# Performance work log

Measured on AMD Instinct MI355X. Metric: run time of the kernel, lower is better.

Reference implementation:

```python
import jax, jax.numpy as jnp
import numpy as np

N, E, D, H, FF = 50000, 1600000, 128, 8, 512
DK = D // H
EPS = 1e-5


def _layernorm(x, g, b):
    mu = jnp.mean(x, axis=-1, keepdims=True)
    var = jnp.mean((x - mu) ** 2, axis=-1, keepdims=True)
    return (x - mu) * jax.lax.rsqrt(var + EPS) * g + b


def setup_inputs() -> dict:
    key = jax.random.key(0)
    ks = jax.random.split(key, 10)
    s = 0.05
    return {
        "h": jax.random.normal(ks[0], (N, D), jnp.float32),
        "src": jax.random.randint(ks[1], (E,), 0, N, jnp.int32),
        "dst": jax.random.randint(ks[2], (E,), 0, N, jnp.int32),
        "Wq": jax.random.normal(ks[3], (D, D), jnp.float32) * s,
        "Wk": jax.random.normal(ks[4], (D, D), jnp.float32) * s,
        "Wv": jax.random.normal(ks[5], (D, D), jnp.float32) * s,
        "Wo": jax.random.normal(ks[6], (D, D), jnp.float32) * s,
        "ln1_g": jnp.ones((D,), jnp.float32),
        "ln1_b": jnp.zeros((D,), jnp.float32),
        "ln2_g": jnp.ones((D,), jnp.float32),
        "ln2_b": jnp.zeros((D,), jnp.float32),
        "W1": jax.random.normal(ks[7], (D, FF), jnp.float32) * s,
        "b1": jnp.zeros((FF,), jnp.float32),
        "W2": jax.random.normal(ks[8], (FF, D), jnp.float32) * s,
        "b2": jnp.zeros((D,), jnp.float32),
    }


def reference(h, src, dst, Wq, Wk, Wv, Wo, ln1_g, ln1_b, ln2_g, ln2_b, W1, b1, W2, b2):
    # QKV projections (bias-free, as in the torch module)
    q = (h @ Wq).reshape(N, H, DK)
    k = (h @ Wk).reshape(N, H, DK)
    v = (h @ Wv).reshape(N, H, DK)

    # masked_mm: per-edge, per-head score  e[m,h] = q[dst[m]] . k[src[m]]
    e = jnp.einsum("ehd,ehd->eh", q[dst], k[src]) / np.sqrt(DK)

    # sparse_softmax: segment softmax over incoming edges of each dst node
    m = jax.ops.segment_max(e, dst, num_segments=N)  # [N, H]
    ex = jnp.exp(e - m[dst])
    denom = jax.ops.segment_sum(ex, dst, num_segments=N)  # [N, H]
    alpha = ex / denom[dst]  # [E, H]

    # vec_spmm: a[n] = sum_{edges m with dst[m]==n} alpha[m] * v[src[m]]
    a = jax.ops.segment_sum(alpha[:, :, None] * v[src], dst, num_segments=N)
    a = a.reshape(N, D)

    o = a @ Wo
    h1 = _layernorm(h + o, ln1_g, ln1_b)
    ffn = jax.nn.relu(h1 @ W1 + b1) @ W2 + b2
    h2 = _layernorm(h1 + ffn, ln2_g, ln2_b)
    return h2
```

## Files before the change

kernel.cpp:

```cpp
#include <hip/hip_runtime.h>
#include <hip/hip_bf16.h>
#include <math.h>

#define D   128
#define FFD 512
#define NPART 8
#define BINB 1024
#define BCAP 768
#define NPROD 32
#define NSUB 32
#define RCAP 320

typedef __attribute__((ext_vector_type(8))) short bf16x8;
typedef __attribute__((ext_vector_type(4))) float f32x4;
typedef __attribute__((ext_vector_type(2))) float f32x2;

static inline size_t align256(size_t x){ return (x + 255) & ~(size_t)255; }

__device__ __forceinline__ float bf2f(unsigned short u){
    union { unsigned int i; float f; } x; x.i = ((unsigned int)u) << 16; return x.f;
}
__device__ __forceinline__ unsigned short f2bf(float f){
    return __builtin_bit_cast(unsigned short, __float2bfloat16(f));
}
__device__ __forceinline__ unsigned char f2fp8(float f){
    return (unsigned char)(__builtin_amdgcn_cvt_pk_fp8_f32(f, f, 0, false) & 0xff);
}

#define DPP_ADD(x, ctrl) do { \
    int yi_ = __builtin_amdgcn_update_dpp(0, __builtin_bit_cast(int, x), ctrl, 0xf, 0xf, true); \
    x += __builtin_bit_cast(float, yi_); } while(0)

__global__ __launch_bounds__(256) void k_bin3(const int* __restrict__ src,
                                              const int* __restrict__ dst, int E, int N,
                                              unsigned long long* __restrict__ pairs,
                                              int* __restrict__ lens,
                                              unsigned long long* __restrict__ spill,
                                              int* __restrict__ qspill){
    __shared__ int lcur[8];
    int tid = threadIdx.x;
    if (tid < 8) lcur[tid] = 0;
    __syncthreads();
    int slice = (N + 7) >> 3;
    int T = gridDim.x * 256;
    unsigned long long* myreg = pairs + (size_t)blockIdx.x * 8 * BCAP;
    for (int i = blockIdx.x*256 + tid; i < E; i += T){
        int d = __builtin_nontemporal_load(&dst[i]);
        int s = __builtin_nontemporal_load(&src[i]);
        int b = min(d / slice, 7);
        unsigned long long pr = ((unsigned long long)(unsigned)d << 32) | (unsigned)s;
        int slot = atomicAdd(&lcur[b], 1);
        if (slot < BCAP) myreg[(size_t)b*BCAP + slot] = pr;
        else { int p = atomicAdd(qspill, 1); spill[p] = pr; }
    }
    __syncthreads();
    if (tid < 8) lens[blockIdx.x*8 + tid] = min(lcur[tid], BCAP);
}

__global__ __launch_bounds__(256) void k_rebin(const unsigned long long* __restrict__ pairs,
                                               const int* __restrict__ lens,
                                               unsigned* __restrict__ pairs2,
                                               int* __restrict__ rlens,
                                               unsigned long long* __restrict__ spill,
                                               int* __restrict__ qspill, int N){
    __shared__ int lcur[NSUB];
    int part = blockIdx.x & 7, ip = blockIdx.x >> 3;
    int tid = threadIdx.x;
    if (tid < NSUB) lcur[tid] = 0;
    __syncthreads();
    int slice = (N + 7) >> 3;
    unsigned subslice = (unsigned)(slice + NSUB - 1) / NSUB;
    int lo_part = part * slice;
    unsigned* outbase = pairs2 + (size_t)(part*NPROD + ip) * NSUB * RCAP;
    for (int seg = ip*(BINB/NPROD); seg < (ip+1)*(BINB/NPROD); ++seg){
        int len = lens[seg*8 + part];
        const unsigned long long* pp = pairs + ((size_t)seg*8 + part)*BCAP;
        for (int i = tid; i < len; i += 256){
            unsigned long long pr = pp[i];
            int d = (int)(pr >> 32);
            unsigned dl = (unsigned)(d - lo_part);
            unsigned sb = dl / subslice;
            int slot = atomicAdd(&lcur[sb], 1);
            if (slot < RCAP)
                outbase[(size_t)sb*RCAP + slot] = ((dl - sb*subslice) << 24) | (unsigned)pr & 0xFFFFFFu;
            else { int p = atomicAdd(qspill, 1); spill[p] = pr; }
        }
    }
    __syncthreads();
    if (tid < NSUB) rlens[(part*NPROD + ip)*NSUB + tid] = min(lcur[tid], RCAP);
}

__global__ __launch_bounds__(256) void k_count4(const unsigned* __restrict__ pairs2,
                                                const int* __restrict__ rlens,
                                                const unsigned long long* __restrict__ spill,
                                                const int* __restrict__ qspill,
                                                int* __restrict__ cnt, int N){
    __shared__ int hist[256];
    int part = blockIdx.x & 7, s = blockIdx.x >> 3;
    int slice = (N + 7) >> 3;
    int subslice = (slice + NSUB - 1) / NSUB;
    int lo_part = part*slice;
    int lo = lo_part + s*subslice;
    int part_end = min(lo_part + slice, N);
    int n_sub = max(0, min(subslice, part_end - lo));
    for (int i = threadIdx.x; i < 256; i += 256) hist[i] = 0;
    __syncthreads();
    for (int ip = 0; ip < NPROD; ++ip){
        int r = (part*NPROD + ip)*NSUB + s;
        int len = rlens[r];
        const unsigned* pp = pairs2 + (size_t)r*RCAP;
        for (int i = threadIdx.x; i < len; i += 256)
            atomicAdd(&hist[pp[i] >> 24], 1);
    }
    int ns = *qspill;
    for (int i = threadIdx.x; i < ns; i += 256){
        int r = (int)(spill[i] >> 32) - lo;
        if (r >= 0 && r < n_sub) atomicAdd(&hist[r], 1);
    }
    __syncthreads();
    for (int i = threadIdx.x; i < n_sub; i += 256) cnt[lo + i] = hist[i];
}

__global__ __launch_bounds__(256) void k_scatter4(const unsigned* __restrict__ pairs2,
                                                  const int* __restrict__ rlens,
                                                  const unsigned long long* __restrict__ spill,
                                                  const int* __restrict__ qspill,
                                                  const int* __restrict__ off,
                                                  int* __restrict__ csr_src, int N){
    __shared__ int curl[256];
    int part = blockIdx.x & 7, s = blockIdx.x >> 3;
    int slice = (N + 7) >> 3;
    int subslice = (slice + NSUB - 1) / NSUB;
    int lo_part = part*slice;
    int lo = lo_part + s*subslice;
    int part_end = min(lo_part + slice, N);
    int n_sub = max(0, min(subslice, part_end - lo));
    for (int i = threadIdx.x; i < n_sub; i += 256) curl[i] = off[lo + i];
    __syncthreads();
    for (int ip = 0; ip < NPROD; ++ip){
        int r = (part*NPROD + ip)*NSUB + s;
        int len = rlens[r];
        const unsigned* pp = pairs2 + (size_t)r*RCAP;
        for (int i = threadIdx.x; i < len; i += 256){
            unsigned e = pp[i];
            int pos = atomicAdd(&curl[e >> 24], 1);
            csr_src[pos] = (int)(e & 0xFFFFFFu);
        }
    }
    int ns = *qspill;
    for (int i = threadIdx.x; i < ns; i += 256){
        unsigned long long pr = spill[i];
        int r = (int)(pr >> 32) - lo;
        if (r >= 0 && r < n_sub){
            int pos = atomicAdd(&curl[r], 1);
            csr_src[pos] = (int)(unsigned)pr;
        }
    }
}

__global__ __launch_bounds__(256) void k_bsum(const int* __restrict__ cnt, int N,
                                              int* __restrict__ bsum){
    int id = blockIdx.x*256 + threadIdx.x;
    int v = (id < N) ? cnt[id] : 0;
    #pragma unroll
    for (int o = 1; o < 64; o <<= 1) v += __shfl_xor(v, o);
    __shared__ int w4[4];
    if ((threadIdx.x & 63) == 0) w4[threadIdx.x >> 6] = v;
    __syncthreads();
    if (threadIdx.x == 0) bsum[blockIdx.x] = w4[0] + w4[1] + w4[2] + w4[3];
}

__global__ __launch_bounds__(1024) void k_scanb(const int* __restrict__ bsum, int NB,
                                                int* __restrict__ ebase,
                                                int* __restrict__ off, int N){
    __shared__ int sh[1024];
    int tid = threadIdx.x;
    int v = (tid < NB) ? bsum[tid] : 0;
    sh[tid] = v; __syncthreads();
    for (int o = 1; o < 1024; o <<= 1){
        int t = (tid >= o) ? sh[tid-o] : 0;
        __syncthreads();
        sh[tid] += t;
        __syncthreads();
    }
    if (tid < NB) ebase[tid] = sh[tid] - v;
    if (tid == NB-1) off[N] = sh[tid];
}

__global__ __launch_bounds__(256) void k_off(const int* __restrict__ cnt, int N,
                                             const int* __restrict__ ebase,
                                             int* __restrict__ off){
    __shared__ int sh[256];
    int tid = threadIdx.x;
    int id = blockIdx.x*256 + tid;
    int v = (id < N) ? cnt[id] : 0;
    sh[tid] = v; __syncthreads();
    for (int o = 1; o < 256; o <<= 1){
        int t = (tid >= o) ? sh[tid-o] : 0;
        __syncthreads();
        sh[tid] += t;
        __syncthreads();
    }
    int excl = sh[tid] - v;
    int base = ebase[blockIdx.x];
    if (id < N) off[id] = base + excl;
}

__global__ __launch_bounds__(256) void k_cast(const float* __restrict__ x,
                                              __hip_bfloat16* __restrict__ y, int n4){
    int i = blockIdx.x*blockDim.x + threadIdx.x;
    if (i >= n4) return;
    float4 f = ((const float4*)x)[i];
    ushort4 u;
    u.x = f2bf(f.x); u.y = f2bf(f.y);
    u.z = f2bf(f.z); u.w = f2bf(f.w);
    ((ushort4*)y)[i] = u;
}

__global__ __launch_bounds__(256) void k_prep_all(
    const float* __restrict__ Wq, const float* __restrict__ Wk,
    const float* __restrict__ Wv, const float* __restrict__ Wo,
    const float* __restrict__ W1, const float* __restrict__ W2,
    __hip_bfloat16* __restrict__ Wqkvt, __hip_bfloat16* __restrict__ Wot,
    __hip_bfloat16* __restrict__ W1t,   __hip_bfloat16* __restrict__ W2t){
    const float* W; __hip_bfloat16* Wt; int K, Nc;
    int y = blockIdx.y;
    switch (y){
        case 0: W = Wq; Wt = Wqkvt; K = 128; Nc = 128; break;
        case 1: W = Wk; Wt = Wqkvt; K = 128; Nc = 128; break;
        case 2: W = Wv; Wt = Wqkvt; K = 128; Nc = 128; break;
        case 3: W = Wo; Wt = Wot;   K = 128; Nc = 128; break;
        case 4: W = W1; Wt = W1t;   K = 128; Nc = 512; break;
        default: W = W2; Wt = W2t;  K = 512; Nc = 128; break;
    }
    int total = K*Nc;
    for (int id = blockIdx.x*256 + threadIdx.x; id < total; id += 256*gridDim.x){
        int n = id / K, kk = id % K;
        size_t drow;
        if (y == 1)      drow = 128 + 8*(n>>2) + (n&3);
        else if (y == 2) drow = 128 + 8*(n>>2) + 4 + (n&3);
        else             drow = n;
        Wt[drow*K + kk] = __float2bfloat16(W[(size_t)kk*Nc + n]);
    }
}

#define BM 128
#define BN 128
#define BK 64

__device__ __forceinline__ bool tile_coords(int M, int &r0, int &c0){
    int ncols = gridDim.x;
    int f = blockIdx.y * ncols + blockIdx.x;
    int xcd = f & 7, s = f >> 3;
    int c = s % ncols, rl = s / ncols;
    int r = rl*8 + xcd;
    r0 = r*BM; c0 = c*BN;
    return r0 < M;
}

__device__ __forceinline__ void stage_tile(const __hip_bfloat16* __restrict__ src,
                                           int row_base, int row_limit, int ldK, int k0,
                                           __hip_bfloat16* lds){
    int tid = threadIdx.x;
    int wave = tid >> 6;
    #pragma unroll
    for (int i = 0; i < 4; ++i){
        int c = i*256 + tid;
        int r = c >> 3, s = c & 7;
        int sg = s ^ (r & 7);
        int gr = row_base + r; if (gr >= row_limit) gr = row_limit - 1;
        const __hip_bfloat16* gp = src + (size_t)gr*ldK + k0 + sg*8;
        char* lp = (char*)lds + (i*256 + wave*64)*16;
        __builtin_amdgcn_global_load_lds((const __attribute__((address_space(1))) void*)gp,
                                         (__attribute__((address_space(3))) void*)lp,
                                         16, 0, 0);
    }
}

__device__ __forceinline__ void stage_rows64(const __hip_bfloat16* __restrict__ src,
                                             int row_base, int ldK, int k0,
                                             __hip_bfloat16* lds){
    int tid = threadIdx.x;
    int wave = tid >> 6;
    #pragma unroll
    for (int i = 0; i < 2; ++i){
        int c = i*256 + tid;
        int r = c >> 3, s = c & 7;
        int sg = s ^ (r & 7);
        const __hip_bfloat16* gp = src + (size_t)(row_base + r)*ldK + k0 + sg*8;
        char* lp = (char*)lds + (i*256 + wave*64)*16;
        __builtin_amdgcn_global_load_lds((const __attribute__((address_space(1))) void*)gp,
                                         (__attribute__((address_space(3))) void*)lp,
                                         16, 0, 0);
    }
}

__device__ __forceinline__ bf16x8 frag(const __hip_bfloat16* buf, int R, int kk, int ls){
    int sl = (kk*4 + ls) ^ (R & 7);
    return *(const bf16x8*)((const char*)buf + R*128 + sl*16);
}

__global__ __launch_bounds__(256) void k_gemm_qkv(
    const __hip_bfloat16* __restrict__ A,
    const __hip_bfloat16* __restrict__ Bt,
    int M,
    __hip_bfloat16* __restrict__ qb, unsigned char* __restrict__ kvq){
    __shared__ __hip_bfloat16 As[BM*BK];
    __shared__ __hip_bfloat16 Bs[BN*BK];
    int r0, c0;
    if (!tile_coords(M, r0, c0)) return;
    int tid = threadIdx.x;
    int lane = tid & 63, wave = tid >> 6;
    int wr = wave >> 1, wc = wave & 1;
    int lr = lane & 15, ls = lane >> 4;

    f32x4 acc[4][4];
    #pragma unroll
    for (int m = 0; m < 4; m++)
        #pragma unroll
        for (int n = 0; n < 4; n++) acc[m][n] = (f32x4){0.f,0.f,0.f,0.f};

    for (int k0 = 0; k0 < 128; k0 += BK){
        stage_tile(A,  r0, M,   128, k0, As);
        stage_tile(Bt, c0, 384, 128, k0, Bs);
        __syncthreads();
        #pragma unroll
        for (int kk = 0; kk < 2; ++kk){
            bf16x8 af[4], bfg[4];
            #pragma unroll
            for (int m = 0; m < 4; m++) af[m]  = frag(As, wr*64 + m*16 + lr, kk, ls);
            #pragma unroll
            for (int n = 0; n < 4; n++) bfg[n] = frag(Bs, wc*64 + n*16 + lr, kk, ls);
            #pragma unroll
            for (int m = 0; m < 4; m++)
                #pragma unroll
                for (int n = 0; n < 4; n++)
                    acc[m][n] = __builtin_amdgcn_mfma_f32_16x16x32_bf16(af[m], bfg[n], acc[m][n], 0, 0, 0);
        }
        __syncthreads();
    }

    int region = c0 >> 7;
    #pragma unroll
    for (int n = 0; n < 4; n++){
        int c16 = wc*64 + n*16 + lr;
        #pragma unroll
        for (int m = 0; m < 4; m++){
            #pragma unroll
            for (int j = 0; j < 4; j++){
                int row = r0 + wr*64 + m*16 + ls*4 + j;
                if (row >= M) continue;
                float v = acc[m][n][j];
                if (region == 0)
                    ((unsigned short*)qb)[(size_t)row*128 + c16] = f2bf(v);
                else
                    kvq[(size_t)row*256 + (region-1)*128 + c16] = f2fp8(v);
            }
        }
    }
}

__global__ __launch_bounds__(256) void k_tail(
    const __hip_bfloat16* __restrict__ ab, const float* __restrict__ h,
    const __hip_bfloat16* __restrict__ Wot,
    const float* __restrict__ ln1g, const float* __restrict__ ln1b,
    const __hip_bfloat16* __restrict__ W1t, const float* __restrict__ b1,
    const __hip_bfloat16* __restrict__ W2t, const float* __restrict__ b2,
    const float* __restrict__ ln2g, const float* __restrict__ ln2b,
    float* __restrict__ out, int M){
    __shared__ __hip_bfloat16 buf0[BM*BK];
    __shared__ __hip_bfloat16 buf1[BM*BK];
    __shared__ __hip_bfloat16 h1s[2][BM*BK];
    __shared__ float red[2][BM][2];
    int f = blockIdx.x;
    int r0 = ((f >> 3)*8 + (f & 7)) * BM;
    if (r0 >= M) return;
    int tid = threadIdx.x;
    int lane = tid & 63, wave = tid >> 6;
    int wr = wave >> 1, wc = wave & 1;
    int lr = lane & 15, ls = lane >> 4;

    f32x4 acc[4][4];
    #pragma unroll
    for (int m = 0; m < 4; m++)
        #pragma unroll
        for (int n = 0; n < 4; n++) acc[m][n] = (f32x4){0.f,0.f,0.f,0.f};

    for (int k0 = 0; k0 < 128; k0 += BK){
        stage_tile(ab,  r0, M,   128, k0, buf0);
        stage_tile(Wot, 0,  128, 128, k0, buf1);
        __syncthreads();
        #pragma unroll
        for (int kk = 0; kk < 2; ++kk){
            bf16x8 af[4], bfg[4];
            #pragma unroll
            for (int m = 0; m < 4; m++) af[m]  = frag(buf0, wr*64 + m*16 + lr, kk, ls);
            #pragma unroll
            for (int n = 0; n < 4; n++) bfg[n] = frag(buf1, wc*64 + n*16 + lr, kk, ls);
            #pragma unroll
            for (int m = 0; m < 4; m++)
                #pragma unroll
                for (int n = 0; n < 4; n++)
                    acc[m][n] = __builtin_amdgcn_mfma_f32_16x16x32_bf16(af[m], bfg[n], acc[m][n], 0, 0, 0);
        }
        __syncthreads();
    }

    #pragma unroll
    for (int m = 0; m < 4; m++){
        #pragma unroll
        for (int j = 0; j < 4; j++){
            int rowl = wr*64 + m*16 + ls*4 + j;
            int row = r0 + rowl;
            float s = 0.f, q = 0.f;
            #pragma unroll
            for (int n = 0; n < 4; n++){
                int col = wc*64 + n*16 + lr;
                float rv = (row < M) ? h[(size_t)row*128 + col] : 0.f;
                float v = acc[m][n][j] + rv;
                acc[m][n][j] = v;
                s += v; q += v*v;
            }
            #pragma unroll
            for (int o = 1; o < 16; o <<= 1){
                s += __shfl_xor(s, o);
                q += __shfl_xor(q, o);
            }
            if (lr == 0){
                red[0][rowl][wc] = s;
                red[1][rowl][wc] = q;
            }
        }
    }
    __syncthreads();
    #pragma unroll
    for (int m = 0; m < 4; m++){
        #pragma unroll
        for (int j = 0; j < 4; j++){
            int rowl = wr*64 + m*16 + ls*4 + j;
            float mu  = (red[0][rowl][0] + red[0][rowl][1]) * (1.f/128.f);
            float eq  = (red[1][rowl][0] + red[1][rowl][1]) * (1.f/128.f);
            float var = fmaxf(eq - mu*mu, 0.f);
            float inv = rsqrtf(var + 1e-5f);
            #pragma unroll
            for (int n = 0; n < 4; n++){
                int col = wc*64 + n*16 + lr;
                float o = (acc[m][n][j] - mu)*inv*ln1g[col] + ln1b[col];
                int hh = col >> 6, c6 = col & 63;
                int slot = (c6 >> 3) ^ (rowl & 7), elem = c6 & 7;
                ((unsigned short*)h1s[hh])[rowl*64 + slot*8 + elem] = f2bf(o);
            }
        }
    }
    __syncthreads();

    f32x4 yacc[4][4];
    #pragma unroll
    for (int m = 0; m < 4; m++)
        #pragma unroll
        for (int n = 0; n < 4; n++) yacc[m][n] = (f32x4){0.f,0.f,0.f,0.f};

    for (int c = 0; c < 8; ++c){
        stage_rows64(W1t, c*64, 128, 0,  buf1);
        stage_rows64(W1t, c*64, 128, 64, buf1 + 64*64);
        __syncthreads();
        f32x4 tacc[4][2];
        #pragma unroll
        for (int m = 0; m < 4; m++)
            #pragma unroll
            for (int n = 0; n < 2; n++) tacc[m][n] = (f32x4){0.f,0.f,0.f,0.f};
        #pragma unroll
        for (int step = 0; step < 2; ++step){
            #pragma unroll
            for (int kk = 0; kk < 2; ++kk){
                bf16x8 af[4], bfg[2];
                #pragma unroll
                for (int m = 0; m < 4; m++) af[m]  = frag(h1s[step], wr*64 + m*16 + lr, kk, ls);
                #pragma unroll
                for (int n = 0; n < 2; n++) bfg[n] = frag(buf1 + step*64*64, wc*32 + n*16 + lr, kk, ls);
                #pragma unroll
                for (int m = 0; m < 4; m++)
                    #pragma unroll
                    for (int n = 0; n < 2; n++)
                        tacc[m][n] = __builtin_amdgcn_mfma_f32_16x16x32_bf16(af[m], bfg[n], tacc[m][n], 0, 0, 0);
            }
        }
        #pragma unroll
        for (int m = 0; m < 4; m++){
            #pragma unroll
            for (int j = 0; j < 4; j++){
                int rowl = wr*64 + m*16 + ls*4 + j;
                #pragma unroll
                for (int n = 0; n < 2; n++){
                    int cc = wc*32 + n*16 + lr;
                    float v = fmaxf(tacc[m][n][j] + b1[c*64 + cc], 0.f);
                    int slot = (cc >> 3) ^ (rowl & 7), elem = cc & 7;
                    ((unsigned short*)buf0)[rowl*64 + slot*8 + elem] = f2bf(v);
                }
            }
        }
        __syncthreads();
        stage_tile(W2t, 0, 128, 512, c*64, buf1);
        __syncthreads();
        #pragma unroll
        for (int kk = 0; kk < 2; ++kk){
            bf16x8 af[4], bfg[4];
            #pragma unroll
            for (int m = 0; m < 4; m++) af[m]  = frag(buf0, wr*64 + m*16 + lr, kk, ls);
            #pragma unroll
            for (int n = 0; n < 4; n++) bfg[n] = frag(buf1, wc*64 + n*16 + lr, kk, ls);
            #pragma unroll
            for (int m = 0; m < 4; m++)
                #pragma unroll
                for (int n = 0; n < 4; n++)
                    yacc[m][n] = __builtin_amdgcn_mfma_f32_16x16x32_bf16(af[m], bfg[n], yacc[m][n], 0, 0, 0);
        }
        __syncthreads();
    }

    #pragma unroll
    for (int m = 0; m < 4; m++){
        #pragma unroll
        for (int j = 0; j < 4; j++){
            int rowl = wr*64 + m*16 + ls*4 + j;
            float s = 0.f, q = 0.f;
            #pragma unroll
            for (int n = 0; n < 4; n++){
                int col = wc*64 + n*16 + lr;
                int hh = col >> 6, c6 = col & 63;
                int slot = (c6 >> 3) ^ (rowl & 7), elem = c6 & 7;
                float h1v = bf2f(((const unsigned short*)h1s[hh])[rowl*64 + slot*8 + elem]);
                float v = yacc[m][n][j] + b2[col] + h1v;
                yacc[m][n][j] = v;
                s += v; q += v*v;
            }
            #pragma unroll
            for (int o = 1; o < 16; o <<= 1){
                s += __shfl_xor(s, o);
                q += __shfl_xor(q, o);
            }
            if (lr == 0){
                red[0][rowl][wc] = s;
                red[1][rowl][wc] = q;
            }
        }
    }
    __syncthreads();
    #pragma unroll
    for (int m = 0; m < 4; m++){
        #pragma unroll
        for (int j = 0; j < 4; j++){
            int rowl = wr*64 + m*16 + ls*4 + j;
            int row = r0 + rowl;
            if (row >= M) continue;
            float mu  = (red[0][rowl][0] + red[0][rowl][1]) * (1.f/128.f);
            float eq  = (red[1][rowl][0] + red[1][rowl][1]) * (1.f/128.f);
            float var = fmaxf(eq - mu*mu, 0.f);
            float inv = rsqrtf(var + 1e-5f);
            #pragma unroll
            for (int n = 0; n < 4; n++){
                int col = wc*64 + n*16 + lr;
                out[(size_t)row*128 + col] = (yacc[m][n][j] - mu)*inv*ln2g[col] + ln2b[col];
            }
        }
    }
}

#define PAIR(jj, dd, b0, b1, b2, b3) { \
    int s0_ = __builtin_amdgcn_readlane(myidx, (jj)); \
    int s1_ = __builtin_amdgcn_readlane(myidx, (jj)+1); \
    int sv_ = half ? s1_ : s0_; \
    uint2 u_ = kv[(size_t)(unsigned)sv_*32 + l32]; \
    f32x2 k01 = __builtin_amdgcn_cvt_pk_f32_fp8((int)u_.x, false); \
    f32x2 k23 = __builtin_amdgcn_cvt_pk_f32_fp8((int)u_.x, true); \
    f32x2 v01 = __builtin_amdgcn_cvt_pk_f32_fp8((int)u_.y, false); \
    f32x2 v23 = __builtin_amdgcn_cvt_pk_f32_fp8((int)u_.y, true); \
    float p_ = q0*k01[0] + q1*k01[1] + q2*k23[0] + q3*k23[1]; \
    DPP_ADD(p_, 0xB1); DPP_ADD(p_, 0x4E); \
    float w_ = __builtin_amdgcn_exp2f(p_); \
    dd += w_; \
    b0 = fmaf(w_, v01[0], b0); b1 = fmaf(w_, v01[1], b1); \
    b2 = fmaf(w_, v23[0], b2); b3 = fmaf(w_, v23[1], b3); }

#define PAIRV(jj, dd, b0, b1, b2, b3) { \
    int s0_ = __builtin_amdgcn_readlane(myidx, (jj)); \
    int s1_ = __builtin_amdgcn_readlane(myidx, min((jj)+1, 63)); \
    int sv_ = half ? s1_ : s0_; \
    uint2 u_ = kv[(size_t)(unsigned)sv_*32 + l32]; \
    f32x2 k01 = __builtin_amdgcn_cvt_pk_f32_fp8((int)u_.x, false); \
    f32x2 k23 = __builtin_amdgcn_cvt_pk_f32_fp8((int)u_.x, true); \
    f32x2 v01 = __builtin_amdgcn_cvt_pk_f32_fp8((int)u_.y, false); \
    f32x2 v23 = __builtin_amdgcn_cvt_pk_f32_fp8((int)u_.y, true); \
    float p_ = q0*k01[0] + q1*k01[1] + q2*k23[0] + q3*k23[1]; \
    DPP_ADD(p_, 0xB1); DPP_ADD(p_, 0x4E); \
    float w_ = __builtin_amdgcn_exp2f(p_); \
    if ((jj) + half >= cnt) w_ = 0.f; \
    dd += w_; \
    b0 = fmaf(w_, v01[0], b0); b1 = fmaf(w_, v01[1], b1); \
    b2 = fmaf(w_, v23[0], b2); b3 = fmaf(w_, v23[1], b3); }

__global__ __launch_bounds__(256) void k_attn(const __hip_bfloat16* __restrict__ qb,
                                              const uint2* __restrict__ kv,
                                              const int* __restrict__ off,
                                              const int* __restrict__ csr_src,
                                              __hip_bfloat16* __restrict__ a, int N){
    int wid = (blockIdx.x*blockDim.x + threadIdx.x) >> 6;
    int lane = threadIdx.x & 63;
    if (wid >= N) return;
    int half = lane >> 5, l32 = lane & 31;
    ushort4 qu = ((const ushort4*)(qb + (size_t)wid*128))[l32];
    const float SC = 0.25f * 1.44269504f;
    float q0 = bf2f(qu.x)*SC, q1 = bf2f(qu.y)*SC, q2 = bf2f(qu.z)*SC, q3 = bf2f(qu.w)*SC;
    int beg = off[wid], end = off[wid+1];
    float dA=0, a0A=0, a1A=0, a2A=0, a3A=0;
    float dB=0, a0B=0, a1B=0, a2B=0, a3B=0;
    for (int e0 = beg; e0 < end; e0 += 64){
        int myidx = (e0 + lane < end) ? csr_src[e0 + lane] : 0;
        int cnt = min(64, end - e0);
        int j = 0;
        for (; j + 3 < cnt; j += 4){
            PAIR(j,   dA, a0A, a1A, a2A, a3A);
            PAIR(j+2, dB, a0B, a1B, a2B, a3B);
        }
        for (; j < cnt; j += 2){
            PAIRV(j, dA, a0A, a1A, a2A, a3A);
        }
    }
    float d  = dA + dB;
    float a0 = a0A + a0B, a1 = a1A + a1B, a2 = a2A + a2B, a3 = a3A + a3B;
    d  += __shfl_xor(d, 32);
    a0 += __shfl_xor(a0, 32);
    a1 += __shfl_xor(a1, 32);
    a2 += __shfl_xor(a2, 32);
    a3 += __shfl_xor(a3, 32);
    if (half == 0){
        float r = (d > 0.f) ? 1.f/d : 0.f;
        ushort4 o;
        o.x = f2bf(a0*r); o.y = f2bf(a1*r); o.z = f2bf(a2*r); o.w = f2bf(a3*r);
        ((ushort4*)(a + (size_t)wid*128))[l32] = o;
    }
}

extern "C" void kernel_launch(void* const* d_in, const int* in_sizes, int n_in,
                              void* d_out, int out_size, void* d_ws, size_t ws_size,
                              hipStream_t stream){
    const float* h    = (const float*)d_in[0];
    const int*   src  = (const int*)  d_in[1];
    const int*   dst  = (const int*)  d_in[2];
    const float* Wq   = (const float*)d_in[3];
    const float* Wk   = (const float*)d_in[4];
    const float* Wv   = (const float*)d_in[5];
    const float* Wo   = (const float*)d_in[6];
    const float* ln1g = (const float*)d_in[7];
    const float* ln1b = (const float*)d_in[8];
    const float* ln2g = (const float*)d_in[9];
    const float* ln2b = (const float*)d_in[10];
    const float* W1   = (const float*)d_in[11];
    const float* b1   = (const float*)d_in[12];
    const float* W2   = (const float*)d_in[13];
    const float* b2   = (const float*)d_in[14];
    float* out = (float*)d_out;

    const int N = in_sizes[0] / D;
    const int E = in_sizes[1];

    char* ws = (char*)d_ws;
    size_t o = 0;
    const size_t row_bf = align256((size_t)N * D * sizeof(__hip_bfloat16));
    const size_t kv_q   = align256((size_t)N * 256);

    __hip_bfloat16* qb  = (__hip_bfloat16*)(ws + o); o += row_bf;
    unsigned char* kvq  = (unsigned char*)(ws + o); o += kv_q;
    __hip_bfloat16* ab  = (__hip_bfloat16*)(ws + o); o += row_bf;
    __hip_bfloat16* hb  = (__hip_bfloat16*)(ws + o); o += row_bf;
    __hip_bfloat16* Wqkvt = (__hip_bfloat16*)(ws + o); o += align256(384*128*2);
    __hip_bfloat16* W1t   = (__hip_bfloat16*)(ws + o); o += align256(512*128*2);
    __hip_bfloat16* W2t   = (__hip_bfloat16*)(ws + o); o += align256(128*512*2);
    __hip_bfloat16* Wot   = (__hip_bfloat16*)(ws + o); o += align256(128*128*2);
    int* cnt   = (int*)(ws + o); o += align256((size_t)N*4);
    int* offp  = (int*)(ws + o); o += align256((size_t)(N+1)*4);
    int* bsum  = (int*)(ws + o); o += align256(1024*4);
    int* ebase = (int*)(ws + o); o += align256(1024*4);
    int* lens  = (int*)(ws + o); o += align256((size_t)BINB*8*4);
    int* rlens = (int*)(ws + o); o += align256((size_t)NPART*NPROD*NSUB*4);
    int* qspill= (int*)(ws + o); o += align256(256);
    int* csr   = (int*)(ws + o); o += align256((size_t)E*4);
    unsigned long long* pairs = (unsigned long long*)(ws + o);
    o += align256((size_t)BINB * 8 * BCAP * 8);
    unsigned* pairs2 = (unsigned*)(ws + o);
    o += align256((size_t)NPART * NPROD * NSUB * RCAP * 4);
    unsigned long long* spill = (unsigned long long*)(ws + o);
    o += align256((size_t)E * 8);

    const int NB = (N + 255)/256;

    (void)hipMemsetAsync(qspill, 0, 256, stream);
    k_bin3<<<BINB, 256, 0, stream>>>(src, dst, E, N, pairs, lens, spill, qspill);

    k_cast<<<(N*D/4 + 255)/256, 256, 0, stream>>>(h, hb, N*D/4);
    k_prep_all<<<dim3(64, 6), 256, 0, stream>>>(Wq, Wk, Wv, Wo, W1, W2,
                                                Wqkvt, Wot, W1t, W2t);

    k_rebin<<<NPART*NPROD, 256, 0, stream>>>(pairs, lens, pairs2, rlens, spill, qspill, N);
    k_count4<<<NPART*NSUB, 256, 0, stream>>>(pairs2, rlens, spill, qspill, cnt, N);
    k_bsum <<<NB, 256, 0, stream>>>(cnt, N, bsum);
    k_scanb<<<1, 1024, 0, stream>>>(bsum, NB, ebase, offp, N);
    k_off  <<<NB, 256, 0, stream>>>(cnt, N, ebase, offp);
    k_scatter4<<<NPART*NSUB, 256, 0, stream>>>(pairs2, rlens, spill, qspill, offp, csr, N);

    int mb = (N + BM - 1)/BM;
    int mb_pad = ((mb + 7)/8)*8;

    k_gemm_qkv<<<dim3(3, mb_pad), 256, 0, stream>>>(hb, Wqkvt, N, qb, kvq);

    k_attn<<<(N*64 + 255)/256, 256, 0, stream>>>(qb, (const uint2*)kvq, offp, csr, ab, N);

    k_tail<<<mb_pad, 256, 0, stream>>>(ab, h, Wot, ln1g, ln1b,
                                       W1t, b1, W2t, b2, ln2g, ln2b, out, N);
}
```

Baseline: 235.3 us.

## Use 512-thread blocks in fused tail kernel with 8-wave column split

The fused tail kernel (Wo projection, LayerNorm, FFN, LayerNorm) moves from 4 waves to 8 waves per 128-row block. Each wave now owns 32 output columns, or 16 FFN hidden columns, instead of twice that, and the row-statistic reductions combine four partial sums per row. Shared memory is merged into one 64KB buffer, with the reduction scratch aliased onto the first staging buffer, and the staging helpers are rewritten for 512 threads. The aim is more waves in flight to hide latency and smaller per-wave accumulators. The cost is that each wave reuses its A-fragments across fewer MFMAs and the same LDS fragment loads are repeated across more waves.

```diff
diff --git a/kernel.cpp b/kernel.cpp
--- a/kernel.cpp
+++ b/kernel.cpp
@@ -277,22 +277,38 @@
     }
 }
 
-__device__ __forceinline__ void stage_rows64(const __hip_bfloat16* __restrict__ src,
-                                             int row_base, int ldK, int k0,
-                                             __hip_bfloat16* lds){
+__device__ __forceinline__ void stage_tile512(const __hip_bfloat16* __restrict__ src,
+                                              int row_base, int row_limit, int ldK, int k0,
+                                              __hip_bfloat16* lds){
     int tid = threadIdx.x;
     int wave = tid >> 6;
     #pragma unroll
     for (int i = 0; i < 2; ++i){
-        int c = i*256 + tid;
+        int c = i*512 + tid;
         int r = c >> 3, s = c & 7;
         int sg = s ^ (r & 7);
-        const __hip_bfloat16* gp = src + (size_t)(row_base + r)*ldK + k0 + sg*8;
-        char* lp = (char*)lds + (i*256 + wave*64)*16;
+        int gr = row_base + r; if (gr >= row_limit) gr = row_limit - 1;
+        const __hip_bfloat16* gp = src + (size_t)gr*ldK + k0 + sg*8;
+        char* lp = (char*)lds + (i*512 + wave*64)*16;
         __builtin_amdgcn_global_load_lds((const __attribute__((address_space(1))) void*)gp,
                                          (__attribute__((address_space(3))) void*)lp,
                                          16, 0, 0);
     }
+}
+
+__device__ __forceinline__ void stage_rows64_512(const __hip_bfloat16* __restrict__ src,
+                                                 int row_base, int ldK, int k0,
+                                                 __hip_bfloat16* lds){
+    int tid = threadIdx.x;
+    int wave = tid >> 6;
+    int c = tid;
+    int r = c >> 3, s = c & 7;
+    int sg = s ^ (r & 7);
+    const __hip_bfloat16* gp = src + (size_t)(row_base + r)*ldK + k0 + sg*8;
+    char* lp = (char*)lds + (wave*64)*16;
+    __builtin_amdgcn_global_load_lds((const __attribute__((address_space(1))) void*)gp,
+                                     (__attribute__((address_space(3))) void*)lp,
+                                     16, 0, 0);
 }
 
 __device__ __forceinline__ bf16x8 frag(const __hip_bfloat16* buf, int R, int kk, int ls){
@@ -360,7 +376,7 @@
     }
 }
 
-__global__ __launch_bounds__(256) void k_tail(
+__global__ __launch_bounds__(512) void k_tail(
     const __hip_bfloat16* __restrict__ ab, const float* __restrict__ h,
     const __hip_bfloat16* __restrict__ Wot,
     const float* __restrict__ ln1g, const float* __restrict__ ln1b,
@@ -368,39 +384,42 @@
     const __hip_bfloat16* __restrict__ W2t, const float* __restrict__ b2,
     const float* __restrict__ ln2g, const float* __restrict__ ln2b,
     float* __restrict__ out, int M){
-    __shared__ __hip_bfloat16 buf0[BM*BK];
-    __shared__ __hip_bfloat16 buf1[BM*BK];
-    __shared__ __hip_bfloat16 h1s[2][BM*BK];
-    __shared__ float red[2][BM][2];
+    __shared__ char smem[65536];
+    __hip_bfloat16* buf0 = (__hip_bfloat16*)smem;
+    __hip_bfloat16* buf1 = (__hip_bfloat16*)(smem + 16384);
+    __hip_bfloat16* h1s0 = (__hip_bfloat16*)(smem + 32768);
+    __hip_bfloat16* h1s1 = (__hip_bfloat16*)(smem + 49152);
+    float* red0 = (float*)smem;
+    float* red1 = (float*)(smem + 2048);
     int f = blockIdx.x;
     int r0 = ((f >> 3)*8 + (f & 7)) * BM;
     if (r0 >= M) return;
     int tid = threadIdx.x;
     int lane = tid & 63, wave = tid >> 6;
-    int wr = wave >> 1, wc = wave & 1;
+    int wr = wave >> 2, wq = wave & 3;
     int lr = lane & 15, ls = lane >> 4;
 
-    f32x4 acc[4][4];
+    f32x4 acc[4][2];
     #pragma unroll
     for (int m = 0; m < 4; m++)
         #pragma unroll
-        for (int n = 0; n < 4; n++) acc[m][n] = (f32x4){0.f,0.f,0.f,0.f};
+        for (int n = 0; n < 2; n++) acc[m][n] = (f32x4){0.f,0.f,0.f,0.f};
 
     for (int k0 = 0; k0 < 128; k0 += BK){
-        stage_tile(ab,  r0, M,   128, k0, buf0);
-        stage_tile(Wot, 0,  128, 128, k0, buf1);
+        stage_tile512(ab,  r0, M,   128, k0, buf0);
+        stage_tile512(Wot, 0,  128, 128, k0, buf1);
         __syncthreads();
         #pragma unroll
         for (int kk = 0; kk < 2; ++kk){
-            bf16x8 af[4], bfg[4];
+            bf16x8 af[4], bfg[2];
             #pragma unroll
             for (int m = 0; m < 4; m++) af[m]  = frag(buf0, wr*64 + m*16 + lr, kk, ls);
             #pragma unroll
-            for (int n = 0; n < 4; n++) bfg[n] = frag(buf1, wc*64 + n*16 + lr, kk, ls);
+            for (int n = 0; n < 2; n++) bfg[n] = frag(buf1, wq*32 + n*16 + lr, kk, ls);
             #pragma unroll
             for (int m = 0; m < 4; m++)
                 #pragma unroll
-                for (int n = 0; n < 4; n++)
+                for (int n = 0; n < 2; n++)
                     acc[m][n] = __builtin_amdgcn_mfma_f32_16x16x32_bf16(af[m], bfg[n], acc[m][n], 0, 0, 0);
         }
         __syncthreads();
@@ -414,8 +433,8 @@
             int row = r0 + rowl;
             float s = 0.f, q = 0.f;
             #pragma unroll
-            for (int n = 0; n < 4; n++){
-                int col = wc*64 + n*16 + lr;
+            for (int n = 0; n < 2; n++){
+                int col = wq*32 + n*16 + lr;
                 float rv = (row < M) ? h[(size_t)row*128 + col] : 0.f;
                 float v = acc[m][n][j] + rv;
                 acc[m][n][j] = v;
@@ -427,8 +446,8 @@
                 q += __shfl_xor(q, o);
             }
             if (lr == 0){
-                red[0][rowl][wc] = s;
-                red[1][rowl][wc] = q;
+                red0[rowl*4 + wq] = s;
+                red1[rowl*4 + wq] = q;
             }
         }
     }
@@ -438,51 +457,49 @@
         #pragma unroll
         for (int j = 0; j < 4; j++){
             int rowl = wr*64 + m*16 + ls*4 + j;
-            float mu  = (red[0][rowl][0] + red[0][rowl][1]) * (1.f/128.f);
-            float eq  = (red[1][rowl][0] + red[1][rowl][1]) * (1.f/128.f);
-            float var = fmaxf(eq - mu*mu, 0.f);
+            float s4 = red0[rowl*4+0] + red0[rowl*4+1] + red0[rowl*4+2] + red0[rowl*4+3];
+            float q4 = red1[rowl*4+0] + red1[rowl*4+1] + red1[rowl*4+2] + red1[rowl*4+3];
+            float mu  = s4 * (1.f/128.f);
+            float var = fmaxf(q4 * (1.f/128.f) - mu*mu, 0.f);
             float inv = rsqrtf(var + 1e-5f);
             #pragma unroll
-            for (int n = 0; n < 4; n++){
-                int col = wc*64 + n*16 + lr;
+            for (int n = 0; n < 2; n++){
+                int col = wq*32 + n*16 + lr;
                 float o = (acc[m][n][j] - mu)*inv*ln1g[col] + ln1b[col];
-                int hh = col >> 6, c6 = col & 63;
+                int c6 = col & 63;
                 int slot = (c6 >> 3) ^ (rowl & 7), elem = c6 & 7;
-                ((unsigned short*)h1s[hh])[rowl*64 + slot*8 + elem] = f2bf(o);
-            }
-        }
-    }
-    __syncthreads();
-
-    f32x4 yacc[4][4];
+                unsigned short* dstp = (unsigned short*)((col >> 6) ? h1s1 : h1s0);
+                dstp[rowl*64 + slot*8 + elem] = f2bf(o);
+            }
+        }
+    }
+    __syncthreads();
+
+    f32x4 yacc[4][2];
     #pragma unroll
     for (int m = 0; m < 4; m++)
         #pragma unroll
-        for (int n = 0; n < 4; n++) yacc[m][n] = (f32x4){0.f,0.f,0.f,0.f};
+        for (int n = 0; n < 2; n++) yacc[m][n] = (f32x4){0.f,0.f,0.f,0.f};
 
     for (int c = 0; c < 8; ++c){
-        stage_rows64(W1t, c*64, 128, 0,  buf1);
-        stage_rows64(W1t, c*64, 128, 64, buf1 + 64*64);
-        __syncthreads();
-        f32x4 tacc[4][2];
-        #pragma unroll
-        for (int m = 0; m < 4; m++)
-            #pragma unroll
-            for (int n = 0; n < 2; n++) tacc[m][n] = (f32x4){0.f,0.f,0.f,0.f};
+        stage_rows64_512(W1t, c*64, 128, 0,  buf1);
+        stage_rows64_512(W1t, c*64, 128, 64, buf1 + 64*64);
+        __syncthreads();
+        f32x4 tacc[4];
+        #pragma unroll
+        for (int m = 0; m < 4; m++) tacc[m] = (f32x4){0.f,0.f,0.f,0.f};
         #pragma unroll
         for (int step = 0; step < 2; ++step){
+            const __hip_bfloat16* hs = step ? h1s1 : h1s0;
             #pragma unroll
             for (int kk = 0; kk < 2; ++kk){
-                bf16x8 af[4], bfg[2];
+                bf16x8 af[4], bw;
                 #pragma unroll
-                for (int m = 0; m < 4; m++) af[m]  = frag(h1s[step], wr*64 + m*16 + lr, kk, ls);
-                #pragma unroll
-                for (int n = 0; n < 2; n++) bfg[n] = frag(buf1 + step*64*64, wc*32 + n*16 + lr, kk, ls);
+                for (int m = 0; m < 4; m++) af[m] = frag(hs, wr*64 + m*16 + lr, kk, ls);
+                bw = frag(buf1 + step*64*64, wq*16 + lr, kk, ls);
                 #pragma unroll
                 for (int m = 0; m < 4; m++)
-                    #pragma unroll
-                    for (int n = 0; n < 2; n++)
-                        tacc[m][n] = __builtin_amdgcn_mfma_f32_16x16x32_bf16(af[m], bfg[n], tacc[m][n], 0, 0, 0);
+                    tacc[m] = __builtin_amdgcn_mfma_f32_16x16x32_bf16(af[m], bw, tacc[m], 0, 0, 0);
             }
         }
         #pragma unroll
@@ -490,29 +507,26 @@
             #pragma unroll
             for (int j = 0; j < 4; j++){
                 int rowl = wr*64 + m*16 + ls*4 + j;
-                #pragma unroll
-                for (int n = 0; n < 2; n++){
-                    int cc = wc*32 + n*16 + lr;
-                    float v = fmaxf(tacc[m][n][j] + b1[c*64 + cc], 0.f);
-                    int slot = (cc >> 3) ^ (rowl & 7), elem = cc & 7;
-                    ((unsigned short*)buf0)[rowl*64 + slot*8 + elem] = f2bf(v);
-                }
-            }
-        }
-        __syncthreads();
-        stage_tile(W2t, 0, 128, 512, c*64, buf1);
+                int cc = wq*16 + lr;
+                float v = fmaxf(tacc[m][j] + b1[c*64 + cc], 0.f);
+                int slot = (cc >> 3) ^ (rowl & 7), elem = cc & 7;
+                ((unsigned short*)buf0)[rowl*64 + slot*8 + elem] = f2bf(v);
+            }
+        }
+        __syncthreads();
+        stage_tile512(W2t, 0, 128, 512, c*64, buf1);
         __syncthreads();
         #pragma unroll
         for (int kk = 0; kk < 2; ++kk){
-            bf16x8 af[4], bfg[4];
+            bf16x8 af[4], bfg[2];
             #pragma unroll
             for (int m = 0; m < 4; m++) af[m]  = frag(buf0, wr*64 + m*16 + lr, kk, ls);
             #pragma unroll
-            for (int n = 0; n < 4; n++) bfg[n] = frag(buf1, wc*64 + n*16 + lr, kk, ls);
+            for (int n = 0; n < 2; n++) bfg[n] = frag(buf1, wq*32 + n*16 + lr, kk, ls);
             #pragma unroll
             for (int m = 0; m < 4; m++)
                 #pragma unroll
-                for (int n = 0; n < 4; n++)
+                for (int n = 0; n < 2; n++)
                     yacc[m][n] = __builtin_amdgcn_mfma_f32_16x16x32_bf16(af[m], bfg[n], yacc[m][n], 0, 0, 0);
         }
         __syncthreads();
@@ -525,11 +539,12 @@
             int rowl = wr*64 + m*16 + ls*4 + j;
             float s = 0.f, q = 0.f;
             #pragma unroll
-            for (int n = 0; n < 4; n++){
-                int col = wc*64 + n*16 + lr;
-                int hh = col >> 6, c6 = col & 63;
+            for (int n = 0; n < 2; n++){
+                int col = wq*32 + n*16 + lr;
+                int c6 = col & 63;
                 int slot = (c6 >> 3) ^ (rowl & 7), elem = c6 & 7;
-                float h1v = bf2f(((const unsigned short*)h1s[hh])[rowl*64 + slot*8 + elem]);
+                const unsigned short* hp = (const unsigned short*)((col >> 6) ? h1s1 : h1s0);
+                float h1v = bf2f(hp[rowl*64 + slot*8 + elem]);
                 float v = yacc[m][n][j] + b2[col] + h1v;
                 yacc[m][n][j] = v;
                 s += v; q += v*v;
@@ -540,8 +555,8 @@
                 q += __shfl_xor(q, o);
             }
             if (lr == 0){
-                red[0][rowl][wc] = s;
-                red[1][rowl][wc] = q;
+                red0[rowl*4 + wq] = s;
+                red1[rowl*4 + wq] = q;
             }
         }
     }
@@ -553,13 +568,14 @@
             int rowl = wr*64 + m*16 + ls*4 + j;
             int row = r0 + rowl;
             if (row >= M) continue;
-            float mu  = (red[0][rowl][0] + red[0][rowl][1]) * (1.f/128.f);
-            float eq  = (red[1][rowl][0] + red[1][rowl][1]) * (1.f/128.f);
-            float var = fmaxf(eq - mu*mu, 0.f);
+            float s4 = red0[rowl*4+0] + red0[rowl*4+1] + red0[rowl*4+2] + red0[rowl*4+3];
+            float q4 = red1[rowl*4+0] + red1[rowl*4+1] + red1[rowl*4+2] + red1[rowl*4+3];
+            float mu  = s4 * (1.f/128.f);
+            float var = fmaxf(q4 * (1.f/128.f) - mu*mu, 0.f);
             float inv = rsqrtf(var + 1e-5f);
             #pragma unroll
-            for (int n = 0; n < 4; n++){
-                int col = wc*64 + n*16 + lr;
+            for (int n = 0; n < 2; n++){
+                int col = wq*32 + n*16 + lr;
                 out[(size_t)row*128 + col] = (yacc[m][n][j] - mu)*inv*ln2g[col] + ln2b[col];
             }
         }
@@ -715,6 +731,6 @@
 
     k_attn<<<(N*64 + 255)/256, 256, 0, stream>>>(qb, (const uint2*)kvq, offp, csr, ab, N);
 
-    k_tail<<<mb_pad, 256, 0, stream>>>(ab, h, Wot, ln1g, ln1b,
+    k_tail<<<mb_pad, 512, 0, stream>>>(ab, h, Wot, ln1g, ln1b,
                                        W1t, b1, W2t, b2, ln2g, ln2b, out, N);
 }
```

Result: faster. 222.5 us (-5.4%).
